# Kernel tuning notes

Hardware: AMD Instinct MI355X
Metric: run time of the kernel (lower is better)

The kernel has to match this reference:

```python
import jax, jax.numpy as jnp
import numpy as np


def setup_inputs() -> dict:
    key = jax.random.key(0)
    k1, k2, k3, k4 = jax.random.split(key, 4)
    B, T, C, H = 16, 2048, 384, 64
    x = jax.random.normal(k1, (B, T, C), dtype=jnp.float32)
    Wq = jax.random.normal(k2, (C, H), dtype=jnp.float32) * (1.0 / np.sqrt(C))
    Wk = jax.random.normal(k3, (C, H), dtype=jnp.float32) * (1.0 / np.sqrt(C))
    Wv = jax.random.normal(k4, (C, H), dtype=jnp.float32) * (1.0 / np.sqrt(C))
    return {"x": x, "Wq": Wq, "Wk": Wk, "Wv": Wv}


def reference(x, Wq, Wk, Wv):
    # x: [B, T, C]; Wq/Wk/Wv: [C, H]
    T = x.shape[1]
    H = Wk.shape[1]
    q = jnp.einsum('btc,ch->bth', x, Wq)
    k = jnp.einsum('btc,ch->bth', x, Wk)
    v = jnp.einsum('btc,ch->bth', x, Wv)
    scale = 1.0 / jnp.sqrt(jnp.asarray(H, dtype=x.dtype))
    wei = jnp.einsum('bth,bsh->bts', q, k) * scale  # [B, T, T]
    causal = jnp.tril(jnp.ones((T, T), dtype=bool))
    wei = jnp.where(causal, wei, -jnp.inf)
    attn = jax.nn.softmax(wei, axis=-1)
    # dropout p=0 -> identity
    out = jnp.einsum('bts,bsh->bth', attn, v)  # [B, T, H]
    return out
```

## Files before the change

### kernel.cpp

```cpp
#include <hip/hip_runtime.h>
#include <hip/hip_bf16.h>

#define B_ 16
#define T_ 2048
#define C_ 384
#define H_ 64

typedef __attribute__((ext_vector_type(8))) short short8;
typedef __attribute__((ext_vector_type(4))) short short4_t;
typedef __attribute__((ext_vector_type(4))) float floatx4;

static __device__ __forceinline__ short f2bf(float f) {
    unsigned u = __builtin_bit_cast(unsigned, f);
    u += 0x7FFF + ((u >> 16) & 1);
    return (short)(u >> 16);
}
static __device__ __forceinline__ float bf2f(short s) {
    return __builtin_bit_cast(float, ((unsigned)(unsigned short)s) << 16);
}

__global__ void wt_kernel(const float* __restrict__ Wq, const float* __restrict__ Wk,
                          const float* __restrict__ Wv, short* __restrict__ wt2) {
    int idx = blockIdx.x * 256 + threadIdx.x;
    if (idx >= 12 * 12 * 512) return;
    int f = idx >> 9, within = idx & 511;
    int lane = within >> 3, jj = within & 7;
    int nt16 = f / 12, kc32 = f - nt16 * 12;
    int mat = nt16 >> 2, w = nt16 & 3;
    int quad = lane >> 4, l16 = lane & 15;
    int h = w * 16 + l16;
    int c = kc32 * 32 + quad * 8 + jj;
    const float* W = (mat == 0) ? Wq : ((mat == 1) ? Wk : Wv);
    wt2[idx] = f2bf(W[c * H_ + h]);
}

__global__ __launch_bounds__(256) void qkv_kernel(
        const float* __restrict__ x, const short* __restrict__ wt2,
        short* __restrict__ qo, short* __restrict__ ko, short* __restrict__ vto) {
    __shared__ short xs[32 * 392];

    int b = blockIdx.y, t0 = blockIdx.x * 32;
    int tid = threadIdx.x;

    const float* src = x + (size_t)(b * T_ + t0) * C_;
    for (int i = 0; i < 12; i++) {
        int chunk = i * 256 + tid;
        int row = chunk / 96, off = (chunk % 96) * 4;
        float4 f = *(const float4*)&src[row * 384 + off];
        short4_t s4;
        s4.x = f2bf(f.x); s4.y = f2bf(f.y); s4.z = f2bf(f.z); s4.w = f2bf(f.w);
        *(short4_t*)&xs[row * 392 + off] = s4;
    }
    __syncthreads();

    int w = tid >> 6, lane = tid & 63, quad = lane >> 4, l16 = lane & 15;

    floatx4 acc[2][3];
    for (int mt = 0; mt < 2; mt++)
        for (int j = 0; j < 3; j++) acc[mt][j] = (floatx4)0.0f;

    for (int kc = 0; kc < 384; kc += 32) {
        int kc32 = kc >> 5;
        short8 a0 = *(const short8*)&xs[l16 * 392 + kc + quad * 8];
        short8 a1 = *(const short8*)&xs[(16 + l16) * 392 + kc + quad * 8];
        for (int j = 0; j < 3; j++) {
            short8 bf = *(const short8*)&wt2[(((j * 4 + w) * 12) + kc32) * 512 + lane * 8];
            acc[0][j] = __builtin_amdgcn_mfma_f32_16x16x32_bf16(a0, bf, acc[0][j], 0, 0, 0);
            acc[1][j] = __builtin_amdgcn_mfma_f32_16x16x32_bf16(a1, bf, acc[1][j], 0, 0, 0);
        }
    }
    __syncthreads();

    {
        int h = w * 16 + l16;
        for (int j = 0; j < 3; j++)
            for (int mt = 0; mt < 2; mt++)
                for (int r = 0; r < 4; r++) {
                    int tl = mt * 16 + quad * 4 + r;
                    short bv = f2bf(acc[mt][j][r]);
                    if (j == 0)      xs[tl * 72 + h] = bv;
                    else if (j == 1) xs[2304 + tl * 72 + h] = bv;
                    else             xs[4608 + h * 40 + tl] = bv;
                }
    }
    __syncthreads();

    {
        int row = tid >> 3, off = (tid & 7) * 8;
        *(short8*)&qo[(size_t)(b * T_ + t0 + row) * H_ + off] = *(const short8*)&xs[row * 72 + off];
        *(short8*)&ko[(size_t)(b * T_ + t0 + row) * H_ + off] = *(const short8*)&xs[2304 + row * 72 + off];
    }
    {
        int h = tid >> 2, off = (tid & 3) * 8;
        *(short8*)&vto[(size_t)(b * H_ + h) * T_ + t0 + off] = *(const short8*)&xs[4608 + h * 40 + off];
    }
}

#define KVSZ (64 * 72)
#define SLOT_BYTES (16384 + 512)

__global__ __launch_bounds__(256) void attn_seg_kernel(
        const short* __restrict__ q, const short* __restrict__ k,
        const short* __restrict__ vt, float* __restrict__ slots) {
    __shared__ short ks[2 * KVSZ];
    __shared__ short vs[2 * KVSZ];
    __shared__ short ps[4 * 16 * 72];

    int b = blockIdx.y, fid = blockIdx.x, nslot = gridDim.x;
    int tt = 0, cum = 0;
    while (cum + ((2 * tt + 5) >> 2) <= fid) { cum += (2 * tt + 5) >> 2; tt++; }
    int nk = 2 * tt + 2;
    int k0 = (fid - cum) * 4;
    int k1 = min(k0 + 4, nk);

    int tid = threadIdx.x, w = tid >> 6, lane = tid & 63, quad = lane >> 4, l16 = lane & 15;
    int trow0 = tt * 128 + w * 32;

    short8 aq[2][2];
    for (int mt = 0; mt < 2; mt++) {
        const short* qrow = q + (size_t)(b * T_ + trow0 + mt * 16 + l16) * H_;
        aq[mt][0] = *(const short8*)&qrow[quad * 8];
        aq[mt][1] = *(const short8*)&qrow[32 + quad * 8];
    }

    floatx4 o[2][4];
    float lp[2][4];
    for (int mt = 0; mt < 2; mt++)
        for (int i = 0; i < 4; i++) { o[mt][i] = (floatx4)0.0f; lp[mt][i] = 0.f; }

    const short* kb0 = k + (size_t)b * T_ * H_;
    const short* vtb = vt + (size_t)b * H_ * T_;
    short* psw = ps + w * 16 * 72;

    int srow = tid >> 3, soff = (tid & 7) * 8;
    const float C1 = 0.125f * 1.44269504f;
    const float C2 = 12.0f * 1.44269504f;

    {
        const short* kg = kb0 + (size_t)k0 * 64 * H_;
        const short* vg = vtb + k0 * 64;
        short8 a = *(const short8*)&kg[srow * H_ + soff];
        short8 c = *(const short8*)&kg[(srow + 32) * H_ + soff];
        short8 d = *(const short8*)&vg[(size_t)srow * T_ + soff];
        short8 e = *(const short8*)&vg[(size_t)(srow + 32) * T_ + soff];
        *(short8*)&ks[srow * 72 + soff] = a;
        *(short8*)&ks[(srow + 32) * 72 + soff] = c;
        *(short8*)&vs[srow * 72 + soff] = d;
        *(short8*)&vs[(srow + 32) * 72 + soff] = e;
    }
    __syncthreads();

    int p = 0;
    for (int st = k0; st < k1; st++) {
        bool more = (st + 1 < k1);
        short8 pk0, pk1, pv0, pv1;
        if (more) {
            const short* kg = kb0 + (size_t)(st + 1) * 64 * H_;
            const short* vg = vtb + (st + 1) * 64;
            pk0 = *(const short8*)&kg[srow * H_ + soff];
            pk1 = *(const short8*)&kg[(srow + 32) * H_ + soff];
            pv0 = *(const short8*)&vg[(size_t)srow * T_ + soff];
            pv1 = *(const short8*)&vg[(size_t)(srow + 32) * T_ + soff];
        }
        const short* ksp = ks + p * KVSZ;
        const short* vsp = vs + p * KVSZ;
        int s0 = st * 64;

        floatx4 sacc[2][4];
        for (int mt = 0; mt < 2; mt++)
            for (int nt = 0; nt < 4; nt++) sacc[mt][nt] = (floatx4)0.0f;
        for (int nt = 0; nt < 4; nt++) {
            short8 bk0 = *(const short8*)&ksp[(nt * 16 + l16) * 72 + quad * 8];
            short8 bk1 = *(const short8*)&ksp[(nt * 16 + l16) * 72 + 32 + quad * 8];
            sacc[0][nt] = __builtin_amdgcn_mfma_f32_16x16x32_bf16(aq[0][0], bk0, sacc[0][nt], 0, 0, 0);
            sacc[0][nt] = __builtin_amdgcn_mfma_f32_16x16x32_bf16(aq[0][1], bk1, sacc[0][nt], 0, 0, 0);
            sacc[1][nt] = __builtin_amdgcn_mfma_f32_16x16x32_bf16(aq[1][0], bk0, sacc[1][nt], 0, 0, 0);
            sacc[1][nt] = __builtin_amdgcn_mfma_f32_16x16x32_bf16(aq[1][1], bk1, sacc[1][nt], 0, 0, 0);
        }

        bool diag = (st >= 2 * tt);
        for (int mt = 0; mt < 2; mt++)
            for (int nt = 0; nt < 4; nt++) {
                int s_idx = s0 + nt * 16 + l16;
                for (int r = 0; r < 4; r++) {
                    float pv = exp2f(fmaf(sacc[mt][nt][r], C1, -C2));
                    if (diag && (s_idx > trow0 + mt * 16 + quad * 4 + r)) pv = 0.0f;
                    lp[mt][r] += pv;
                    sacc[mt][nt][r] = pv;
                }
            }

        short8 ap[2][2];
        for (int mt = 0; mt < 2; mt++) {
            for (int nt = 0; nt < 4; nt++)
                for (int r = 0; r < 4; r++)
                    psw[(quad * 4 + r) * 72 + nt * 16 + l16] = f2bf(sacc[mt][nt][r]);
            ap[mt][0] = *(const short8*)&psw[l16 * 72 + quad * 8];
            ap[mt][1] = *(const short8*)&psw[l16 * 72 + 32 + quad * 8];
        }

        for (int nh = 0; nh < 4; nh++) {
            short8 bv0 = *(const short8*)&vsp[(nh * 16 + l16) * 72 + quad * 8];
            short8 bv1 = *(const short8*)&vsp[(nh * 16 + l16) * 72 + 32 + quad * 8];
            o[0][nh] = __builtin_amdgcn_mfma_f32_16x16x32_bf16(ap[0][0], bv0, o[0][nh], 0, 0, 0);
            o[0][nh] = __builtin_amdgcn_mfma_f32_16x16x32_bf16(ap[0][1], bv1, o[0][nh], 0, 0, 0);
            o[1][nh] = __builtin_amdgcn_mfma_f32_16x16x32_bf16(ap[1][0], bv0, o[1][nh], 0, 0, 0);
            o[1][nh] = __builtin_amdgcn_mfma_f32_16x16x32_bf16(ap[1][1], bv1, o[1][nh], 0, 0, 0);
        }

        if (more) {
            short* kd = ks + (1 - p) * KVSZ;
            short* vd = vs + (1 - p) * KVSZ;
            *(short8*)&kd[srow * 72 + soff] = pk0;
            *(short8*)&kd[(srow + 32) * 72 + soff] = pk1;
            *(short8*)&vd[srow * 72 + soff] = pv0;
            *(short8*)&vd[(srow + 32) * 72 + soff] = pv1;
            __syncthreads();
            p ^= 1;
        }
    }

    for (int d = 1; d < 16; d <<= 1)
        for (int mt = 0; mt < 2; mt++)
            for (int r = 0; r < 4; r++)
                lp[mt][r] += __shfl_xor(lp[mt][r], d, 16);

    char* slotb = (char*)slots + ((size_t)b * nslot + fid) * SLOT_BYTES;
    short* slotO = (short*)slotb;
    float* slotL = (float*)(slotb + 16384);

    for (int mt = 0; mt < 2; mt++) {
        for (int nh = 0; nh < 4; nh++)
            for (int r = 0; r < 4; r++)
                psw[(quad * 4 + r) * 72 + nh * 16 + l16] = f2bf(o[mt][nh][r]);
        for (int it = 0; it < 2; it++) {
            int u = it * 64 + lane;
            int row = u >> 3, seg = u & 7;
            *(short8*)&slotO[(w * 32 + mt * 16 + row) * 64 + seg * 8] =
                *(const short8*)&psw[row * 72 + seg * 8];
        }
    }
    if (l16 == 0)
        for (int mt = 0; mt < 2; mt++)
            for (int r = 0; r < 4; r++)
                slotL[w * 32 + mt * 16 + quad * 4 + r] = lp[mt][r];
}

__global__ __launch_bounds__(256) void combine_kernel(
        const float* __restrict__ slots, int nslot, float* __restrict__ out) {
    int b = blockIdx.y, tt = blockIdx.x;
    int nseg = (2 * tt + 5) >> 2;
    int cum = 0;
    for (int i = 0; i < tt; i++) cum += (2 * i + 5) >> 2;
    const char* base = (const char*)slots + ((size_t)b * nslot + cum) * SLOT_BYTES;

    int tid = threadIdx.x;
    int row = tid >> 1, half = tid & 1;
    float acc[32];
    for (int i = 0; i < 32; i++) acc[i] = 0.f;
    float lsum = 0.f;
    for (int s = 0; s < nseg; s++) {
        const short* O = (const short*)(base + (size_t)s * SLOT_BYTES);
        const float* L = (const float*)(base + (size_t)s * SLOT_BYTES + 16384);
        for (int i = 0; i < 4; i++) {
            short8 v = *(const short8*)&O[row * 64 + half * 32 + i * 8];
            for (int j = 0; j < 8; j++) acc[i * 8 + j] += bf2f(v[j]);
        }
        lsum += L[row];
    }
    float inv = 1.0f / lsum;
    float* op = out + (size_t)(b * T_ + tt * 128 + row) * H_ + half * 32;
    for (int i = 0; i < 8; i++) {
        float4 v;
        v.x = acc[i * 4 + 0] * inv; v.y = acc[i * 4 + 1] * inv;
        v.z = acc[i * 4 + 2] * inv; v.w = acc[i * 4 + 3] * inv;
        *(float4*)&op[i * 4] = v;
    }
}

template<bool DIAG>
static __device__ __forceinline__ void attn_step(
        int s0, int t0w, int quad, int l16,
        const short* __restrict__ kbase, const short* __restrict__ vtb,
        short8 aq0, short8 aq1, short* __restrict__ psw,
        floatx4 (&o)[4], float (&lpart)[4]) {
    floatx4 sacc[4];
    for (int nt = 0; nt < 4; nt++) sacc[nt] = (floatx4)0.0f;
    for (int nt = 0; nt < 4; nt++) {
        short8 bk0 = *(const short8*)&kbase[(nt * 16 + l16) * H_ + quad * 8];
        short8 bk1 = *(const short8*)&kbase[(nt * 16 + l16) * H_ + 32 + quad * 8];
        sacc[nt] = __builtin_amdgcn_mfma_f32_16x16x32_bf16(aq0, bk0, sacc[nt], 0, 0, 0);
        sacc[nt] = __builtin_amdgcn_mfma_f32_16x16x32_bf16(aq1, bk1, sacc[nt], 0, 0, 0);
    }
    const float C1 = 0.125f * 1.44269504f;
    const float C2 = 12.0f * 1.44269504f;
    for (int nt = 0; nt < 4; nt++) {
        int s_idx = s0 + nt * 16 + l16;
        for (int r = 0; r < 4; r++) {
            float p = exp2f(fmaf(sacc[nt][r], C1, -C2));
            if (DIAG && (s_idx > t0w + quad * 4 + r)) p = 0.0f;
            lpart[r] += p;
            psw[(quad * 4 + r) * 72 + nt * 16 + l16] = f2bf(p);
        }
    }
    short8 ap0 = *(const short8*)&psw[l16 * 72 + quad * 8];
    short8 ap1 = *(const short8*)&psw[l16 * 72 + 32 + quad * 8];
    for (int nh = 0; nh < 4; nh++) {
        short8 bv0 = *(const short8*)&vtb[(size_t)(nh * 16 + l16) * T_ + s0 + quad * 8];
        short8 bv1 = *(const short8*)&vtb[(size_t)(nh * 16 + l16) * T_ + s0 + 32 + quad * 8];
        o[nh] = __builtin_amdgcn_mfma_f32_16x16x32_bf16(ap0, bv0, o[nh], 0, 0, 0);
        o[nh] = __builtin_amdgcn_mfma_f32_16x16x32_bf16(ap1, bv1, o[nh], 0, 0, 0);
    }
}

__global__ __launch_bounds__(256) void attn_kernel(
        const short* __restrict__ q, const short* __restrict__ k,
        const short* __restrict__ vt, float* __restrict__ out) {
    __shared__ short ps[4 * 16 * 72];

    int b = blockIdx.y;
    int g = ((int)blockIdx.x + 4 * (b & 7)) & 31;
    int tt = (b < 8) ? g : 31 - g;
    int t0 = tt * 64;
    int tid = threadIdx.x, w = tid >> 6, lane = tid & 63, quad = lane >> 4, l16 = lane & 15;
    int t0w = t0 + w * 16;

    const short* qrow = q + (size_t)(b * T_ + t0w + l16) * H_;
    short8 aq0 = *(const short8*)&qrow[quad * 8];
    short8 aq1 = *(const short8*)&qrow[32 + quad * 8];

    floatx4 o[4];
    for (int nh = 0; nh < 4; nh++) o[nh] = (floatx4)0.0f;
    float lpart[4] = {0.f, 0.f, 0.f, 0.f};

    const short* kb0 = k + (size_t)b * T_ * H_;
    const short* vtb = vt + (size_t)b * H_ * T_;
    short* psw = ps + w * 16 * 72;

    for (int st = 0; st < tt; st++)
        attn_step<false>(st * 64, t0w, quad, l16, kb0 + (size_t)st * 64 * H_,
                         vtb, aq0, aq1, psw, o, lpart);
    attn_step<true>(tt * 64, t0w, quad, l16, kb0 + (size_t)tt * 64 * H_,
                    vtb, aq0, aq1, psw, o, lpart);

    for (int d = 1; d < 16; d <<= 1)
        for (int r = 0; r < 4; r++)
            lpart[r] += __shfl_xor(lpart[r], d, 16);

    for (int nh = 0; nh < 4; nh++)
        for (int r = 0; r < 4; r++) {
            int t = t0w + quad * 4 + r;
            out[(size_t)(b * T_ + t) * H_ + nh * 16 + l16] = o[nh][r] / lpart[r];
        }
}

extern "C" void kernel_launch(void* const* d_in, const int* in_sizes, int n_in,
                              void* d_out, int out_size, void* d_ws, size_t ws_size,
                              hipStream_t stream) {
    const float* x  = (const float*)d_in[0];
    const float* Wq = (const float*)d_in[1];
    const float* Wk = (const float*)d_in[2];
    const float* Wv = (const float*)d_in[3];

    char* ws = (char*)d_ws;
    short* qb  = (short*)(ws);
    short* kb  = (short*)(ws + (size_t)4 * 1024 * 1024);
    short* vtb = (short*)(ws + (size_t)8 * 1024 * 1024);
    short* wtb = (short*)(ws + (size_t)12 * 1024 * 1024);
    float* slots = (float*)(ws + (size_t)12 * 1024 * 1024 + 256 * 1024);
    size_t base_need = (size_t)12 * 1024 * 1024 + 256 * 1024;

    wt_kernel<<<dim3(288), dim3(256), 0, stream>>>(Wq, Wk, Wv, wtb);
    qkv_kernel<<<dim3(T_ / 32, B_), dim3(256), 0, stream>>>(x, wtb, qb, kb, vtb);

    float* out = (float*)d_out;
    const int NSLOT = 72;
    if (ws_size >= base_need + (size_t)B_ * NSLOT * (size_t)SLOT_BYTES) {
        attn_seg_kernel<<<dim3(NSLOT, B_), dim3(256), 0, stream>>>(qb, kb, vtb, slots);
        combine_kernel<<<dim3(T_ / 128, B_), dim3(256), 0, stream>>>(slots, NSLOT, out);
    } else {
        attn_kernel<<<dim3(T_ / 64, B_), dim3(256), 0, stream>>>(qb, kb, vtb, out);
    }
}
```

Baseline: 140.6 us.

## Compute S transposed so P feeds PV MFMA from registers, skip LDS

Swaps the MFMA operand order for QK^T so each lane holds a column of scores along the key dimension. The softmax probabilities can then be packed directly into bf16 A-operands for 16x16x16 MFMAs, removing the per-wave LDS round trip for P. Row sums reduce across quads with two shuffles instead of four. The output is now written to the slot with scalar bf16 stores instead of being staged through LDS. The trade-off is twice as many smaller MFMAs for PV and narrower global stores.

```diff
diff --git a/kernel.cpp b/kernel.cpp
--- a/kernel.cpp
+++ b/kernel.cpp
@@ -9,6 +9,12 @@
 typedef __attribute__((ext_vector_type(8))) short short8;
 typedef __attribute__((ext_vector_type(4))) short short4_t;
 typedef __attribute__((ext_vector_type(4))) float floatx4;
+
+#if defined(__has_builtin)
+#if __has_builtin(__builtin_amdgcn_mfma_f32_16x16x16bf16_1k)
+#define HAVE_MFMA16 1
+#endif
+#endif
 
 static __device__ __forceinline__ short f2bf(float f) {
     unsigned u = __builtin_bit_cast(unsigned, f);
@@ -104,7 +110,9 @@
         const short* __restrict__ vt, float* __restrict__ slots) {
     __shared__ short ks[2 * KVSZ];
     __shared__ short vs[2 * KVSZ];
+#if !defined(HAVE_MFMA16)
     __shared__ short ps[4 * 16 * 72];
+#endif
 
     int b = blockIdx.y, fid = blockIdx.x, nslot = gridDim.x;
     int tt = 0, cum = 0;
@@ -124,13 +132,12 @@
     }
 
     floatx4 o[2][4];
-    float lp[2][4];
     for (int mt = 0; mt < 2; mt++)
-        for (int i = 0; i < 4; i++) { o[mt][i] = (floatx4)0.0f; lp[mt][i] = 0.f; }
+        for (int i = 0; i < 4; i++) o[mt][i] = (floatx4)0.0f;
+    float lp[2] = {0.f, 0.f};
 
     const short* kb0 = k + (size_t)b * T_ * H_;
     const short* vtb = vt + (size_t)b * H_ * T_;
-    short* psw = ps + w * 16 * 72;
 
     int srow = tid >> 3, soff = (tid & 7) * 8;
     const float C1 = 0.125f * 1.44269504f;
@@ -139,14 +146,10 @@
     {
         const short* kg = kb0 + (size_t)k0 * 64 * H_;
         const short* vg = vtb + k0 * 64;
-        short8 a = *(const short8*)&kg[srow * H_ + soff];
-        short8 c = *(const short8*)&kg[(srow + 32) * H_ + soff];
-        short8 d = *(const short8*)&vg[(size_t)srow * T_ + soff];
-        short8 e = *(const short8*)&vg[(size_t)(srow + 32) * T_ + soff];
-        *(short8*)&ks[srow * 72 + soff] = a;
-        *(short8*)&ks[(srow + 32) * 72 + soff] = c;
-        *(short8*)&vs[srow * 72 + soff] = d;
-        *(short8*)&vs[(srow + 32) * 72 + soff] = e;
+        *(short8*)&ks[srow * 72 + soff] = *(const short8*)&kg[srow * H_ + soff];
+        *(short8*)&ks[(srow + 32) * 72 + soff] = *(const short8*)&kg[(srow + 32) * H_ + soff];
+        *(short8*)&vs[srow * 72 + soff] = *(const short8*)&vg[(size_t)srow * T_ + soff];
+        *(short8*)&vs[(srow + 32) * 72 + soff] = *(const short8*)&vg[(size_t)(srow + 32) * T_ + soff];
     }
     __syncthreads();
 
@@ -172,33 +175,53 @@
         for (int nt = 0; nt < 4; nt++) {
             short8 bk0 = *(const short8*)&ksp[(nt * 16 + l16) * 72 + quad * 8];
             short8 bk1 = *(const short8*)&ksp[(nt * 16 + l16) * 72 + 32 + quad * 8];
-            sacc[0][nt] = __builtin_amdgcn_mfma_f32_16x16x32_bf16(aq[0][0], bk0, sacc[0][nt], 0, 0, 0);
-            sacc[0][nt] = __builtin_amdgcn_mfma_f32_16x16x32_bf16(aq[0][1], bk1, sacc[0][nt], 0, 0, 0);
-            sacc[1][nt] = __builtin_amdgcn_mfma_f32_16x16x32_bf16(aq[1][0], bk0, sacc[1][nt], 0, 0, 0);
-            sacc[1][nt] = __builtin_amdgcn_mfma_f32_16x16x32_bf16(aq[1][1], bk1, sacc[1][nt], 0, 0, 0);
+            sacc[0][nt] = __builtin_amdgcn_mfma_f32_16x16x32_bf16(bk0, aq[0][0], sacc[0][nt], 0, 0, 0);
+            sacc[0][nt] = __builtin_amdgcn_mfma_f32_16x16x32_bf16(bk1, aq[0][1], sacc[0][nt], 0, 0, 0);
+            sacc[1][nt] = __builtin_amdgcn_mfma_f32_16x16x32_bf16(bk0, aq[1][0], sacc[1][nt], 0, 0, 0);
+            sacc[1][nt] = __builtin_amdgcn_mfma_f32_16x16x32_bf16(bk1, aq[1][1], sacc[1][nt], 0, 0, 0);
         }
 
         bool diag = (st >= 2 * tt);
-        for (int mt = 0; mt < 2; mt++)
+#if defined(HAVE_MFMA16)
+        short4_t pa[2][4];
+        for (int mt = 0; mt < 2; mt++) {
+            int q_idx = trow0 + mt * 16 + l16;
             for (int nt = 0; nt < 4; nt++) {
-                int s_idx = s0 + nt * 16 + l16;
+                short4_t pk;
                 for (int r = 0; r < 4; r++) {
                     float pv = exp2f(fmaf(sacc[mt][nt][r], C1, -C2));
-                    if (diag && (s_idx > trow0 + mt * 16 + quad * 4 + r)) pv = 0.0f;
-                    lp[mt][r] += pv;
-                    sacc[mt][nt][r] = pv;
+                    int s_idx = s0 + nt * 16 + quad * 4 + r;
+                    if (diag && (s_idx > q_idx)) pv = 0.0f;
+                    lp[mt] += pv;
+                    pk[r] = f2bf(pv);
                 }
+                pa[mt][nt] = pk;
             }
-
+        }
+        for (int nh = 0; nh < 4; nh++) {
+            const short* vrow = &vsp[(nh * 16 + l16) * 72 + quad * 4];
+            for (int c = 0; c < 4; c++) {
+                short4_t bv = *(const short4_t*)&vrow[c * 16];
+                o[0][nh] = __builtin_amdgcn_mfma_f32_16x16x16bf16_1k(pa[0][c], bv, o[0][nh], 0, 0, 0);
+                o[1][nh] = __builtin_amdgcn_mfma_f32_16x16x16bf16_1k(pa[1][c], bv, o[1][nh], 0, 0, 0);
+            }
+        }
+#else
+        short* psw = ps + w * 16 * 72;
         short8 ap[2][2];
         for (int mt = 0; mt < 2; mt++) {
+            int q_idx = trow0 + mt * 16 + l16;
             for (int nt = 0; nt < 4; nt++)
-                for (int r = 0; r < 4; r++)
-                    psw[(quad * 4 + r) * 72 + nt * 16 + l16] = f2bf(sacc[mt][nt][r]);
+                for (int r = 0; r < 4; r++) {
+                    float pv = exp2f(fmaf(sacc[mt][nt][r], C1, -C2));
+                    int s_idx = s0 + nt * 16 + quad * 4 + r;
+                    if (diag && (s_idx > q_idx)) pv = 0.0f;
+                    lp[mt] += pv;
+                    psw[l16 * 72 + nt * 16 + quad * 4 + r] = f2bf(pv);
+                }
             ap[mt][0] = *(const short8*)&psw[l16 * 72 + quad * 8];
             ap[mt][1] = *(const short8*)&psw[l16 * 72 + 32 + quad * 8];
         }
-
         for (int nh = 0; nh < 4; nh++) {
             short8 bv0 = *(const short8*)&vsp[(nh * 16 + l16) * 72 + quad * 8];
             short8 bv1 = *(const short8*)&vsp[(nh * 16 + l16) * 72 + 32 + quad * 8];
@@ -207,6 +230,7 @@
             o[1][nh] = __builtin_amdgcn_mfma_f32_16x16x32_bf16(ap[1][0], bv0, o[1][nh], 0, 0, 0);
             o[1][nh] = __builtin_amdgcn_mfma_f32_16x16x32_bf16(ap[1][1], bv1, o[1][nh], 0, 0, 0);
         }
+#endif
 
         if (more) {
             short* kd = ks + (1 - p) * KVSZ;
@@ -220,30 +244,22 @@
         }
     }
 
-    for (int d = 1; d < 16; d <<= 1)
-        for (int mt = 0; mt < 2; mt++)
-            for (int r = 0; r < 4; r++)
-                lp[mt][r] += __shfl_xor(lp[mt][r], d, 16);
+    for (int mt = 0; mt < 2; mt++) {
+        lp[mt] += __shfl_xor(lp[mt], 16);
+        lp[mt] += __shfl_xor(lp[mt], 32);
+    }
 
     char* slotb = (char*)slots + ((size_t)b * nslot + fid) * SLOT_BYTES;
     short* slotO = (short*)slotb;
     float* slotL = (float*)(slotb + 16384);
 
-    for (int mt = 0; mt < 2; mt++) {
+    for (int mt = 0; mt < 2; mt++)
         for (int nh = 0; nh < 4; nh++)
             for (int r = 0; r < 4; r++)
-                psw[(quad * 4 + r) * 72 + nh * 16 + l16] = f2bf(o[mt][nh][r]);
-        for (int it = 0; it < 2; it++) {
-            int u = it * 64 + lane;
-            int row = u >> 3, seg = u & 7;
-            *(short8*)&slotO[(w * 32 + mt * 16 + row) * 64 + seg * 8] =
-                *(const short8*)&psw[row * 72 + seg * 8];
-        }
-    }
-    if (l16 == 0)
+                slotO[(w * 32 + mt * 16 + quad * 4 + r) * 64 + nh * 16 + l16] = f2bf(o[mt][nh][r]);
+    if (quad == 0)
         for (int mt = 0; mt < 2; mt++)
-            for (int r = 0; r < 4; r++)
-                slotL[w * 32 + mt * 16 + quad * 4 + r] = lp[mt][r];
+            slotL[w * 32 + mt * 16 + l16] = lp[mt];
 }
 
 __global__ __launch_bounds__(256) void combine_kernel(
```

Measured after the change: 138.9 us. Within noise of the previous version (-1.2%).
